# Kernel tuning notes

Hardware: AMD Instinct MI355X
Metric: run time of the kernel (lower is better)

The kernel has to match this reference:

```python
import jax, jax.numpy as jnp
import numpy as np

K = 1.0      # spring constant
R0 = 1.0     # equilibrium bond length
EPS = 1e-20  # division guard
NUM_GRAPHS = 64


def setup_inputs() -> dict:
    key = jax.random.key(0)
    k1, k2, k3 = jax.random.split(key, 3)
    N, E = 100000, 3200000
    pos = jax.random.normal(k1, (N, 3), dtype=jnp.float32)
    edge_index = jax.random.randint(k2, (2, E), 0, N, dtype=jnp.int64)
    batch = jnp.sort(jax.random.randint(k3, (N,), 0, NUM_GRAPHS, dtype=jnp.int64))
    return {"pos": pos, "edge_index": edge_index, "batch": batch}


def reference(pos, edge_index, batch):
    i, j = edge_index[0], edge_index[1]
    dr = pos[i] - pos[j]                       # (E, 3)
    d = jnp.linalg.norm(dr, axis=1)            # (E,)
    delta = d - R0
    edge_energy = 0.5 * K * delta ** 2         # (E,)
    energy = jax.ops.segment_sum(edge_energy, batch[i], num_segments=NUM_GRAPHS)
    direction = dr / (d + EPS)[:, None]        # (E, 3)
    force_contrib = (K * delta)[:, None] * direction
    forces = jnp.zeros_like(pos).at[i].add(-force_contrib).at[j].add(force_contrib)
    return energy, forces
```

## Files before the change

kernel.cpp:

```cpp
#include <hip/hip_runtime.h>

#define NUM_GRAPHS 64
#define NSC 160
#define SCN 625
#define SCF 1875
#define SCFP 1888
#define SB 512
#define CAP 128
#define SEGSTRIDE (NSC * CAP)
#define PBREC 12800
#define FSCALE 32768.0f
#define FINV   (1.0f / 32768.0f)

__global__ __launch_bounds__(256) void pack_kernel(
    const float* __restrict__ pos, const int* __restrict__ batch,
    float4* __restrict__ pos4, int N)
{
    const int n = blockIdx.x * 256 + threadIdx.x;
    if (n < N) {
        float4 v;
        v.x = pos[3 * n + 0];
        v.y = pos[3 * n + 1];
        v.z = pos[3 * n + 2];
        v.w = __int_as_float(batch[n]);
        pos4[n] = v;
    }
}

__global__ __launch_bounds__(1024, 8) void bin_kernel(
    const int* __restrict__ ei,
    unsigned int* __restrict__ recs,
    int* __restrict__ counts,
    int E, int per_block)
{
    __shared__ unsigned int buf[PBREC];
    __shared__ int hist[NSC];
    __shared__ int csr[NSC];
    __shared__ int cursor[NSC];
    __shared__ int scan_s[NSC];

    const int t = threadIdx.x, b = blockIdx.x;
    const int lane = t & 63, w = t >> 6;
    const int e0 = b * per_block, e1 = min(E, e0 + per_block);

    for (int i = t; i < NSC; i += 1024) hist[i] = 0;
    __syncthreads();

    for (int e = e0 + t; e < e1; e += 1024) {
        const int iv = ei[e], jv = ei[E + e];
        atomicAdd(&hist[iv / SCN], 1);
        atomicAdd(&hist[jv / SCN], 1);
    }
    __syncthreads();

    if (t < NSC) scan_s[t] = hist[t];
    __syncthreads();
    for (int d = 1; d < NSC; d <<= 1) {
        int v = 0;
        if (t < NSC && t >= d) v = scan_s[t - d];
        __syncthreads();
        if (t < NSC) scan_s[t] += v;
        __syncthreads();
    }
    if (t < NSC) {
        const int excl = scan_s[t] - hist[t];
        csr[t] = excl;
        cursor[t] = excl;
    }
    __syncthreads();

    for (int e = e0 + t; e < e1; e += 1024) {
        const int iv = ei[e], jv = ei[E + e];
        const int si = iv / SCN, sj = jv / SCN;
        const int s1 = atomicAdd(&cursor[si], 1);
        buf[s1] = (unsigned int)(iv - si * SCN) | ((unsigned int)jv << 10) | (1u << 27);
        const int s2 = atomicAdd(&cursor[sj], 1);
        buf[s2] = (unsigned int)(jv - sj * SCN) | ((unsigned int)iv << 10);
    }
    __syncthreads();

    unsigned int* dst0 = recs + (size_t)b * NSC * CAP;
    for (int s = w; s < NSC; s += 16) {
        const int base = csr[s];
        const int cnt  = min(hist[s], CAP);
        for (int k = lane; k < cnt; k += 64)
            dst0[s * CAP + k] = buf[base + k];
        if (lane == 0) counts[b * NSC + s] = cnt;
    }
}

template<int G>
__global__ __launch_bounds__(256, 8) void accumulate_kernel(
    const float4* __restrict__ pos4,
    const unsigned int* __restrict__ recs,
    const int* __restrict__ counts,
    float* __restrict__ energy,
    int* __restrict__ partials)
{
    __shared__ float4 slab[SCN];
    __shared__ __align__(16) int facc[SCFP];
    __shared__ float ered[8];

    const int t    = threadIdx.x;
    const int lane = t & 63;
    const int w    = t >> 6;
    const int s    = blockIdx.x % NSC;
    const int g    = blockIdx.x / NSC;

    constexpr int SPB   = SB / G;
    constexpr int SPW   = SPB / 4;
    constexpr int NPASS = (SPW + 7) / 8;

    for (int i = t; i < SCN; i += 256) slab[i] = pos4[s * SCN + i];
    for (int i = 4 * t; i < SCFP; i += 1024) {
        int4 z = {0, 0, 0, 0};
        *(int4*)&facc[i] = z;
    }
    __syncthreads();

    const int gmin_i = __float_as_int(slab[0].w);
    float e_lo = 0.f, e_hi = 0.f;

    for (int pass = 0; pass < NPASS; ++pass) {
        const int seg0 = g * SPB + w * SPW + pass * 8;
        int v = (lane < 8) ? counts[(seg0 + lane) * NSC + s] : 0;
        #pragma unroll
        for (int d = 1; d < 8; d <<= 1) {
            const int u = __shfl_up(v, d);
            if (lane >= d) v += u;
        }
        const int b0 = __shfl(v, 0), b1 = __shfl(v, 1), b2 = __shfl(v, 2),
                  b3 = __shfl(v, 3), b4 = __shfl(v, 4), b5 = __shfl(v, 5),
                  b6 = __shfl(v, 6);
        const int tot = __shfl(v, 7);
        const unsigned int* bp = recs + ((size_t)seg0 * NSC + s) * CAP;

        for (int base = 0; base < tot; base += 256) {
            unsigned int rec[4];
            bool  val[4];
            int   a[4];
            float4 pb[4];
            #pragma unroll
            for (int u = 0; u < 4; ++u) {
                const int r = base + lane + (u << 6);
                val[u] = r < tot;
                if (val[u]) {
                    const int k = (r >= b0) + (r >= b1) + (r >= b2) + (r >= b3)
                                + (r >= b4) + (r >= b5) + (r >= b6);
                    int prev = 0;
                    prev = (k > 0) ? b0 : prev; prev = (k > 1) ? b1 : prev;
                    prev = (k > 2) ? b2 : prev; prev = (k > 3) ? b3 : prev;
                    prev = (k > 4) ? b4 : prev; prev = (k > 5) ? b5 : prev;
                    prev = (k > 6) ? b6 : prev;
                    rec[u] = bp[(size_t)k * SEGSTRIDE + (r - prev)];
                }
            }
            #pragma unroll
            for (int u = 0; u < 4; ++u) {
                if (val[u]) {
                    a[u]  = (int)(rec[u] & 1023);
                    pb[u] = pos4[(rec[u] >> 10) & 0x1FFFF];
                }
            }
            #pragma unroll
            for (int u = 0; u < 4; ++u) {
                if (val[u]) {
                    const float4 pa = slab[a[u]];
                    const float dx = pa.x - pb[u].x;
                    const float dy = pa.y - pb[u].y;
                    const float dz = pa.z - pb[u].z;
                    const float d     = sqrtf(dx*dx + dy*dy + dz*dz);
                    const float delta = d - 1.0f;
                    const float sc    = delta / (d + 1e-20f);
                    const int l = a[u] * 3;
                    atomicAdd(&facc[l + 0], __float2int_rn(-sc * dx * FSCALE));
                    atomicAdd(&facc[l + 1], __float2int_rn(-sc * dy * FSCALE));
                    atomicAdd(&facc[l + 2], __float2int_rn(-sc * dz * FSCALE));
                    if (rec[u] >> 27) {
                        const float e = 0.5f * delta * delta;
                        if (__float_as_int(pa.w) == gmin_i) e_lo += e;
                        else                                e_hi += e;
                    }
                }
            }
        }
    }

    #pragma unroll
    for (int d = 32; d > 0; d >>= 1) {
        e_lo += __shfl_down(e_lo, d);
        e_hi += __shfl_down(e_hi, d);
    }
    if (lane == 0) { ered[2 * w] = e_lo; ered[2 * w + 1] = e_hi; }

    __syncthreads();
    int* dst = partials + (size_t)(s * G + g) * SCFP;
    for (int i = 4 * t; i < SCFP; i += 1024)
        *(int4*)(dst + i) = *(const int4*)&facc[i];
    if (t == 0)
        atomicAdd(&energy[__float_as_int(slab[0].w)],
                  ered[0] + ered[2] + ered[4] + ered[6]);
    if (t == 1)
        atomicAdd(&energy[__float_as_int(slab[SCN - 1].w)],
                  ered[1] + ered[3] + ered[5] + ered[7]);
}

template<int G>
__global__ __launch_bounds__(256) void reduce_kernel(
    const int* __restrict__ partials, float* __restrict__ forces)
{
    const int idx = blockIdx.x * 256 + threadIdx.x;
    if (idx >= NSC * SCF) return;
    const int s = idx / SCF, l = idx - s * SCF;
    int sum = 0;
    #pragma unroll
    for (int g = 0; g < G; ++g)
        sum += partials[(size_t)(s * G + g) * SCFP + l];
    forces[idx] = (float)sum * FINV;
}

extern "C" void kernel_launch(void* const* d_in, const int* in_sizes, int n_in,
                              void* d_out, int out_size, void* d_ws, size_t ws_size,
                              hipStream_t stream) {
    const float* pos   = (const float*)d_in[0];
    const int*   ei    = (const int*)d_in[1];
    const int*   batch = (const int*)d_in[2];

    const int E = in_sizes[1] / 2;
    const int N = in_sizes[0] / 3;

    float* energy = (float*)d_out;
    float* forces = (float*)d_out + NUM_GRAPHS;

    const int per_block = (E + SB - 1) / SB;

    char* w = (char*)d_ws;
    float4* pos4 = (float4*)w;
    size_t off = (size_t)N * 16;
    unsigned int* recs = (unsigned int*)(w + off);
    off += (size_t)SB * NSC * CAP * 4;
    int* counts = (int*)(w + off);
    off += (size_t)SB * NSC * 4;
    int* partials = (int*)(w + off);

    hipMemsetAsync(d_out, 0, NUM_GRAPHS * sizeof(float), stream);

    pack_kernel<<<(N + 255) / 256, 256, 0, stream>>>(pos, batch, pos4, N);

    bin_kernel<<<SB, 1024, 0, stream>>>(ei, recs, counts, E, per_block);

    const size_t need16 = off + (size_t)NSC * 16 * SCFP * sizeof(int);
    if (ws_size >= need16) {
        accumulate_kernel<16><<<NSC * 16, 256, 0, stream>>>(
            pos4, recs, counts, energy, partials);
        reduce_kernel<16><<<(NSC * SCF + 255) / 256, 256, 0, stream>>>(
            partials, forces);
    } else {
        accumulate_kernel<8><<<NSC * 8, 256, 0, stream>>>(
            pos4, recs, counts, energy, partials);
        reduce_kernel<8><<<(NSC * SCF + 255) / 256, 256, 0, stream>>>(
            partials, forces);
    }
}
```

Baseline: 153.1 us.

## Scatter edge records directly to global bins and use rsqrt force math

The bin kernel no longer runs a histogram pass, prefix scan and LDS staging buffer. Each edge now claims a slot with an LDS atomic cursor and writes its record straight to the global per-bin array, dropping anything beyond CAP. This removes a second read of the edge indices and several barriers, but the global writes become scattered instead of coalesced per bin. Separately, the accumulate kernel replaces sqrt plus divide with a hardware reciprocal square root, computing sc = 1 - rsq(r2) and delta = r2*inv - 1, at slightly lower precision.

```diff
diff --git a/kernel.cpp b/kernel.cpp
--- a/kernel.cpp
+++ b/kernel.cpp
@@ -8,7 +8,6 @@
 #define SB 512
 #define CAP 128
 #define SEGSTRIDE (NSC * CAP)
-#define PBREC 12800
 #define FSCALE 32768.0f
 #define FINV   (1.0f / 32768.0f)
 
@@ -33,60 +32,31 @@
     int* __restrict__ counts,
     int E, int per_block)
 {
-    __shared__ unsigned int buf[PBREC];
-    __shared__ int hist[NSC];
-    __shared__ int csr[NSC];
     __shared__ int cursor[NSC];
-    __shared__ int scan_s[NSC];
 
     const int t = threadIdx.x, b = blockIdx.x;
-    const int lane = t & 63, w = t >> 6;
     const int e0 = b * per_block, e1 = min(E, e0 + per_block);
 
-    for (int i = t; i < NSC; i += 1024) hist[i] = 0;
-    __syncthreads();
-
-    for (int e = e0 + t; e < e1; e += 1024) {
-        const int iv = ei[e], jv = ei[E + e];
-        atomicAdd(&hist[iv / SCN], 1);
-        atomicAdd(&hist[jv / SCN], 1);
-    }
-    __syncthreads();
-
-    if (t < NSC) scan_s[t] = hist[t];
-    __syncthreads();
-    for (int d = 1; d < NSC; d <<= 1) {
-        int v = 0;
-        if (t < NSC && t >= d) v = scan_s[t - d];
-        __syncthreads();
-        if (t < NSC) scan_s[t] += v;
-        __syncthreads();
-    }
-    if (t < NSC) {
-        const int excl = scan_s[t] - hist[t];
-        csr[t] = excl;
-        cursor[t] = excl;
-    }
-    __syncthreads();
-
+    for (int i = t; i < NSC; i += 1024) cursor[i] = 0;
+    __syncthreads();
+
+    unsigned int* dst0 = recs + (size_t)b * NSC * CAP;
     for (int e = e0 + t; e < e1; e += 1024) {
         const int iv = ei[e], jv = ei[E + e];
         const int si = iv / SCN, sj = jv / SCN;
         const int s1 = atomicAdd(&cursor[si], 1);
-        buf[s1] = (unsigned int)(iv - si * SCN) | ((unsigned int)jv << 10) | (1u << 27);
+        if (s1 < CAP)
+            dst0[si * CAP + s1] = (unsigned int)(iv - si * SCN)
+                                | ((unsigned int)jv << 10) | (1u << 27);
         const int s2 = atomicAdd(&cursor[sj], 1);
-        buf[s2] = (unsigned int)(jv - sj * SCN) | ((unsigned int)iv << 10);
-    }
-    __syncthreads();
-
-    unsigned int* dst0 = recs + (size_t)b * NSC * CAP;
-    for (int s = w; s < NSC; s += 16) {
-        const int base = csr[s];
-        const int cnt  = min(hist[s], CAP);
-        for (int k = lane; k < cnt; k += 64)
-            dst0[s * CAP + k] = buf[base + k];
-        if (lane == 0) counts[b * NSC + s] = cnt;
-    }
+        if (s2 < CAP)
+            dst0[sj * CAP + s2] = (unsigned int)(jv - sj * SCN)
+                                | ((unsigned int)iv << 10);
+    }
+    __syncthreads();
+
+    for (int i = t; i < NSC; i += 1024)
+        counts[b * NSC + i] = min(cursor[i], CAP);
 }
 
 template<int G>
@@ -169,14 +139,15 @@
                     const float dx = pa.x - pb[u].x;
                     const float dy = pa.y - pb[u].y;
                     const float dz = pa.z - pb[u].z;
-                    const float d     = sqrtf(dx*dx + dy*dy + dz*dz);
-                    const float delta = d - 1.0f;
-                    const float sc    = delta / (d + 1e-20f);
+                    const float r2  = fmaxf(dx*dx + dy*dy + dz*dz, 1e-24f);
+                    const float inv = __builtin_amdgcn_rsqf(r2);
+                    const float sc  = 1.0f - inv;
                     const int l = a[u] * 3;
                     atomicAdd(&facc[l + 0], __float2int_rn(-sc * dx * FSCALE));
                     atomicAdd(&facc[l + 1], __float2int_rn(-sc * dy * FSCALE));
                     atomicAdd(&facc[l + 2], __float2int_rn(-sc * dz * FSCALE));
                     if (rec[u] >> 27) {
+                        const float delta = r2 * inv - 1.0f;
                         const float e = 0.5f * delta * delta;
                         if (__float_as_int(pa.w) == gmin_i) e_lo += e;
                         else                                e_hi += e;
```

Measured after the change: 166.0 us. 1.08x slower.

## Pack y/z fixed-point forces into 64-bit LDS atomics and use rsq

Applied to the files above, without the earlier changes.

Replaces three 32-bit LDS atomics per edge with one 32-bit atomic for x and one 64-bit atomic carrying y and z packed together. Sign borrows between the halves cancel once the two halves are split and summed as 32-bit integers. Also replaces the sqrt-and-divide with a hardware reciprocal square root, computing the scale as 1 - 1/d and the energy delta from r2*inv. The partials layout and the reduce kernel are restructured per node. This cuts LDS atomic count at the cost of rsq precision and a clamp on near-zero distances that changes the EPS guard semantics.

```diff
diff --git a/kernel.cpp b/kernel.cpp
--- a/kernel.cpp
+++ b/kernel.cpp
@@ -4,7 +4,7 @@
 #define NSC 160
 #define SCN 625
 #define SCF 1875
-#define SCFP 1888
+#define XPAD 628
 #define SB 512
 #define CAP 128
 #define SEGSTRIDE (NSC * CAP)
@@ -95,10 +95,12 @@
     const unsigned int* __restrict__ recs,
     const int* __restrict__ counts,
     float* __restrict__ energy,
-    int* __restrict__ partials)
+    int* __restrict__ xpart,
+    unsigned long long* __restrict__ yzpart)
 {
     __shared__ float4 slab[SCN];
-    __shared__ __align__(16) int facc[SCFP];
+    __shared__ __align__(16) int facc_x[XPAD];
+    __shared__ __align__(16) unsigned long long facc_yz[XPAD];
     __shared__ float ered[8];
 
     const int t    = threadIdx.x;
@@ -112,9 +114,13 @@
     constexpr int NPASS = (SPW + 7) / 8;
 
     for (int i = t; i < SCN; i += 256) slab[i] = pos4[s * SCN + i];
-    for (int i = 4 * t; i < SCFP; i += 1024) {
+    for (int i = 4 * t; i < XPAD; i += 1024) {
         int4 z = {0, 0, 0, 0};
-        *(int4*)&facc[i] = z;
+        *(int4*)&facc_x[i] = z;
+    }
+    for (int i = 4 * t; i < 2 * XPAD; i += 1024) {
+        int4 z = {0, 0, 0, 0};
+        *(int4*)&((int*)facc_yz)[i] = z;
     }
     __syncthreads();
 
@@ -169,14 +175,19 @@
                     const float dx = pa.x - pb[u].x;
                     const float dy = pa.y - pb[u].y;
                     const float dz = pa.z - pb[u].z;
-                    const float d     = sqrtf(dx*dx + dy*dy + dz*dz);
-                    const float delta = d - 1.0f;
-                    const float sc    = delta / (d + 1e-20f);
-                    const int l = a[u] * 3;
-                    atomicAdd(&facc[l + 0], __float2int_rn(-sc * dx * FSCALE));
-                    atomicAdd(&facc[l + 1], __float2int_rn(-sc * dy * FSCALE));
-                    atomicAdd(&facc[l + 2], __float2int_rn(-sc * dz * FSCALE));
+                    const float r2  = fmaxf(dx*dx + dy*dy + dz*dz, 1e-24f);
+                    const float inv = __builtin_amdgcn_rsqf(r2);
+                    const float sc  = 1.0f - inv;
+                    const int xq = __float2int_rn(-sc * dx * FSCALE);
+                    const int yq = __float2int_rn(-sc * dy * FSCALE);
+                    const int zq = __float2int_rn(-sc * dz * FSCALE);
+                    atomicAdd(&facc_x[a[u]], xq);
+                    const unsigned long long pk =
+                        ((unsigned long long)(unsigned int)zq << 32)
+                        + (unsigned long long)(unsigned int)yq;
+                    atomicAdd(&facc_yz[a[u]], pk);
                     if (rec[u] >> 27) {
+                        const float delta = r2 * inv - 1.0f;
                         const float e = 0.5f * delta * delta;
                         if (__float_as_int(pa.w) == gmin_i) e_lo += e;
                         else                                e_hi += e;
@@ -194,9 +205,10 @@
     if (lane == 0) { ered[2 * w] = e_lo; ered[2 * w + 1] = e_hi; }
 
     __syncthreads();
-    int* dst = partials + (size_t)(s * G + g) * SCFP;
-    for (int i = 4 * t; i < SCFP; i += 1024)
-        *(int4*)(dst + i) = *(const int4*)&facc[i];
+    int* xdst = xpart + (size_t)(s * G + g) * XPAD;
+    unsigned long long* zdst = yzpart + (size_t)(s * G + g) * XPAD;
+    for (int i = t; i < SCN; i += 256) xdst[i] = facc_x[i];
+    for (int i = t; i < SCN; i += 256) zdst[i] = facc_yz[i];
     if (t == 0)
         atomicAdd(&energy[__float_as_int(slab[0].w)],
                   ered[0] + ered[2] + ered[4] + ered[6]);
@@ -207,16 +219,25 @@
 
 template<int G>
 __global__ __launch_bounds__(256) void reduce_kernel(
-    const int* __restrict__ partials, float* __restrict__ forces)
-{
-    const int idx = blockIdx.x * 256 + threadIdx.x;
-    if (idx >= NSC * SCF) return;
-    const int s = idx / SCF, l = idx - s * SCF;
-    int sum = 0;
+    const int* __restrict__ xpart,
+    const unsigned long long* __restrict__ yzpart,
+    float* __restrict__ forces, int N)
+{
+    const int n = blockIdx.x * 256 + threadIdx.x;
+    if (n >= N) return;
+    const int s = n / SCN, a = n - s * SCN;
+    int sx = 0, sy = 0, sz = 0;
     #pragma unroll
-    for (int g = 0; g < G; ++g)
-        sum += partials[(size_t)(s * G + g) * SCFP + l];
-    forces[idx] = (float)sum * FINV;
+    for (int g = 0; g < G; ++g) {
+        const size_t p = (size_t)(s * G + g) * XPAD + a;
+        sx += xpart[p];
+        const unsigned long long v = yzpart[p];
+        sy += (int)(unsigned int)(v & 0xffffffffull);
+        sz += (int)(unsigned int)(v >> 32);
+    }
+    forces[3 * n + 0] = (float)sx * FINV;
+    forces[3 * n + 1] = (float)sy * FINV;
+    forces[3 * n + 2] = (float)sz * FINV;
 }
 
 extern "C" void kernel_launch(void* const* d_in, const int* in_sizes, int n_in,
@@ -241,7 +262,9 @@
     off += (size_t)SB * NSC * CAP * 4;
     int* counts = (int*)(w + off);
     off += (size_t)SB * NSC * 4;
-    int* partials = (int*)(w + off);
+    int* xpart = (int*)(w + off);
+    const size_t xbytes16 = (size_t)NSC * 16 * XPAD * 4;
+    const size_t xbytes8  = (size_t)NSC * 8  * XPAD * 4;
 
     hipMemsetAsync(d_out, 0, NUM_GRAPHS * sizeof(float), stream);
 
@@ -249,16 +272,18 @@
 
     bin_kernel<<<SB, 1024, 0, stream>>>(ei, recs, counts, E, per_block);
 
-    const size_t need16 = off + (size_t)NSC * 16 * SCFP * sizeof(int);
+    const size_t need16 = off + xbytes16 + (size_t)NSC * 16 * XPAD * 8;
     if (ws_size >= need16) {
+        unsigned long long* yzpart = (unsigned long long*)((char*)xpart + xbytes16);
         accumulate_kernel<16><<<NSC * 16, 256, 0, stream>>>(
-            pos4, recs, counts, energy, partials);
-        reduce_kernel<16><<<(NSC * SCF + 255) / 256, 256, 0, stream>>>(
-            partials, forces);
+            pos4, recs, counts, energy, xpart, yzpart);
+        reduce_kernel<16><<<(N + 255) / 256, 256, 0, stream>>>(
+            xpart, yzpart, forces, N);
     } else {
+        unsigned long long* yzpart = (unsigned long long*)((char*)xpart + xbytes8);
         accumulate_kernel<8><<<NSC * 8, 256, 0, stream>>>(
-            pos4, recs, counts, energy, partials);
-        reduce_kernel<8><<<(NSC * SCF + 255) / 256, 256, 0, stream>>>(
-            partials, forces);
-    }
-}
+            pos4, recs, counts, energy, xpart, yzpart);
+        reduce_kernel<8><<<(N + 255) / 256, 256, 0, stream>>>(
+            xpart, yzpart, forces, N);
+    }
+}
```

Result: faster. 147.2 us (-3.8%).
